# Kernel tuning notes

Measured on AMD Instinct MI355X. Metric: run time of the kernel, lower is better.

Reference implementation:

```python
import jax, jax.numpy as jnp
import numpy as np

DIM = 1024
HEADS = 16
HEAD_DIM = DIM // HEADS
MLP_DIM = 4096
EPS = 1e-12  # F.normalize eps


def l2_rms(x, g):
    # repo RMSNorm: F.normalize(x, dim=-1) * sqrt(d) * g  (g is a scalar param)
    d = x.shape[-1]
    n = jnp.sqrt(jnp.sum(x * x, axis=-1, keepdims=True))
    return x / jnp.maximum(n, EPS) * (d ** 0.5) * g


def setup_inputs() -> dict:
    key = jax.random.key(0)
    ks = jax.random.split(key, 8)
    B, N = 2, 2048
    s = lambda fan_in: 1.0 / np.sqrt(fan_in)
    return {
        "x": jax.random.normal(ks[0], (B, N, DIM), jnp.float32),
        "w_qkv": jax.random.normal(ks[1], (DIM, 3 * DIM), jnp.float32) * s(DIM),
        "b_qkv": jnp.zeros((3 * DIM,), jnp.float32),
        "w_proj": jax.random.normal(ks[2], (DIM, DIM), jnp.float32) * s(DIM),
        "b_proj": jnp.zeros((DIM,), jnp.float32),
        "g_norm1": jnp.ones((1,), jnp.float32),
        "g_norm2": jnp.ones((1,), jnp.float32),
        "g_qnorm": jnp.ones((1,), jnp.float32),
        "g_knorm": jnp.ones((1,), jnp.float32),
        "w_fc1": jax.random.normal(ks[3], (DIM, MLP_DIM), jnp.float32) * s(DIM),
        "b_fc1": jnp.zeros((MLP_DIM,), jnp.float32),
        "w_fc2": jax.random.normal(ks[4], (MLP_DIM, DIM), jnp.float32) * s(MLP_DIM),
        "b_fc2": jnp.zeros((DIM,), jnp.float32),
    }


def reference(x, w_qkv, b_qkv, w_proj, b_proj, g_norm1, g_norm2,
              g_qnorm, g_knorm, w_fc1, b_fc1, w_fc2, b_fc2):
    B, N, D = x.shape
    # --- attention branch ---
    h = l2_rms(x, g_norm1)
    qkv = h @ w_qkv + b_qkv                      # [B,N,3D]
    qkv = qkv.reshape(B, N, 3, HEADS, HEAD_DIM)
    q, k, v = [jnp.transpose(qkv[:, :, i], (0, 2, 1, 3)) for i in range(3)]  # [B,H,N,d]
    q = l2_rms(q, g_qnorm)
    k = l2_rms(k, g_knorm)
    scale = HEAD_DIM ** -0.5
    scores = jnp.einsum('bhqd,bhkd->bhqk', q * scale, k)   # explicit [B,H,N,N]
    attn = jax.nn.softmax(scores, axis=-1)
    o = jnp.einsum('bhqk,bhkd->bhqd', attn, v)
    o = jnp.transpose(o, (0, 2, 1, 3)).reshape(B, N, D)
    x = x + (o @ w_proj + b_proj)
    # --- MLP branch ---
    h = l2_rms(x, g_norm2)
    h = jax.nn.gelu(h @ w_fc1 + b_fc1, approximate=True)
    x = x + (h @ w_fc2 + b_fc2)
    return x
```

## Files before the change

kernel.cpp:

```cpp
#include <hip/hip_runtime.h>
#include <stdint.h>

#define SEQ_ 2048
#define DIM_ 1024
#define HD_ 64
#define NH_ 16

typedef __bf16 bf16x8 __attribute__((ext_vector_type(8)));
typedef float f32x4 __attribute__((ext_vector_type(4)));
typedef __attribute__((address_space(1))) unsigned int as1_uint;
typedef __attribute__((address_space(3))) unsigned int as3_uint;

__device__ __forceinline__ unsigned short f2bf(float f) {
  unsigned u = __builtin_bit_cast(unsigned, f);
  u += 0x7fffu + ((u >> 16) & 1u);
  return (unsigned short)(u >> 16);
}
__device__ __forceinline__ float bf2f(unsigned short u) {
  return __builtin_bit_cast(float, ((unsigned)u) << 16);
}
__device__ __forceinline__ unsigned pk_bf2(float lo, float hi) {
  return __builtin_amdgcn_perm(__builtin_bit_cast(unsigned, hi),
                               __builtin_bit_cast(unsigned, lo), 0x07060302u);
}

__device__ __forceinline__ void gload_lds16(const void* g, void* l) {
  __builtin_amdgcn_global_load_lds(
      reinterpret_cast<as1_uint*>(reinterpret_cast<uintptr_t>(g)),
      reinterpret_cast<as3_uint*>(
          static_cast<unsigned int>(reinterpret_cast<uintptr_t>(l))),
      16, 0, 0);
}

__global__ __launch_bounds__(256) void transpose_cvt(
    const float* __restrict__ W, unsigned short* __restrict__ Wt, int K, int N) {
  __shared__ float t[32][33];
  const int tx = threadIdx.x & 31, ty = threadIdx.x >> 5;
  const int n0 = blockIdx.x * 32, k0 = blockIdx.y * 32;
#pragma unroll
  for (int i = 0; i < 4; i++)
    t[ty + i * 8][tx] = W[(size_t)(k0 + ty + i * 8) * N + n0 + tx];
  __syncthreads();
#pragma unroll
  for (int i = 0; i < 4; i++)
    Wt[(size_t)(n0 + ty + i * 8) * K + k0 + tx] = f2bf(t[tx][ty + i * 8]);
}

__global__ __launch_bounds__(256) void rmsnorm_k(
    const float* __restrict__ x, const float* __restrict__ g,
    unsigned short* __restrict__ out) {
  const int row = blockIdx.x;
  const float4* xr = (const float4*)(x + (size_t)row * DIM_);
  float4 v = xr[threadIdx.x];
  float ss = v.x * v.x + v.y * v.y + v.z * v.z + v.w * v.w;
  ss += __shfl_xor(ss, 1);  ss += __shfl_xor(ss, 2);  ss += __shfl_xor(ss, 4);
  ss += __shfl_xor(ss, 8);  ss += __shfl_xor(ss, 16); ss += __shfl_xor(ss, 32);
  __shared__ float red[4];
  if ((threadIdx.x & 63) == 0) red[threadIdx.x >> 6] = ss;
  __syncthreads();
  float tot = red[0] + red[1] + red[2] + red[3];
  float sc = 32.0f * g[0] / fmaxf(sqrtf(tot), 1e-12f);
  unsigned short* orow = out + (size_t)row * DIM_;
  const int b4 = threadIdx.x * 4;
  orow[b4 + 0] = f2bf(v.x * sc);
  orow[b4 + 1] = f2bf(v.y * sc);
  orow[b4 + 2] = f2bf(v.z * sc);
  orow[b4 + 3] = f2bf(v.w * sc);
}

template <int EPI>
__global__ __launch_bounds__(256, 2) void gemm_bf16(
    const unsigned short* __restrict__ A, const unsigned short* __restrict__ Bt,
    const float* __restrict__ bias, const float* __restrict__ res,
    void* __restrict__ Cout, int M, int N, int K) {
  __shared__ __align__(16) unsigned short As[128 * 32];
  __shared__ __align__(16) unsigned short Bs[128 * 32];
  const int tid = threadIdx.x;
  const int w = tid >> 6, lane = tid & 63;
  const int wm = w >> 1, wn = w & 1;
  const int quad = lane >> 4, l15 = lane & 15;
  const int bn = blockIdx.x, bm = blockIdx.y;
  const int Kchunk = K / gridDim.z;
  const int kbeg = blockIdx.z * Kchunk;

  f32x4 acc[4][4];
#pragma unroll
  for (int i = 0; i < 4; i++)
#pragma unroll
    for (int j = 0; j < 4; j++) acc[i][j] = f32x4{0.f, 0.f, 0.f, 0.f};

  const int r0 = w * 16 + (lane >> 2);
  const int c0 = (lane & 3) * 8;
  const unsigned short* gA0 = A + (size_t)(bm * 128 + r0) * K + kbeg + c0;
  const unsigned short* gA1 = gA0 + (size_t)64 * K;
  const unsigned short* gB0 = Bt + (size_t)(bn * 128 + r0) * K + kbeg + c0;
  const unsigned short* gB1 = gB0 + (size_t)64 * K;
  unsigned short* lA0 = As + w * 512;
  unsigned short* lA1 = As + 2048 + w * 512;
  unsigned short* lB0 = Bs + w * 512;
  unsigned short* lB1 = Bs + 2048 + w * 512;

  for (int kk = 0; kk < Kchunk; kk += 32) {
    gload_lds16(gA0, lA0);
    gload_lds16(gA1, lA1);
    gload_lds16(gB0, lB0);
    gload_lds16(gB1, lB1);
    gA0 += 32; gA1 += 32; gB0 += 32; gB1 += 32;
    __syncthreads();
    bf16x8 af[4], bf[4];
#pragma unroll
    for (int i = 0; i < 4; i++) {
      af[i] = *(const bf16x8*)&As[(wm * 64 + i * 16 + l15) * 32 + quad * 8];
      bf[i] = *(const bf16x8*)&Bs[(wn * 64 + i * 16 + l15) * 32 + quad * 8];
    }
#pragma unroll
    for (int i = 0; i < 4; i++)
#pragma unroll
      for (int j = 0; j < 4; j++)
        acc[i][j] = __builtin_amdgcn_mfma_f32_16x16x32_bf16(af[i], bf[j], acc[i][j], 0, 0, 0);
    __syncthreads();
  }

  const int rowb = bm * 128 + wm * 64;
  const int colb = bn * 128 + wn * 64;
  float* Cz = (float*)Cout + (size_t)blockIdx.z * M * N;
#pragma unroll
  for (int i = 0; i < 4; i++) {
#pragma unroll
    for (int j = 0; j < 4; j++) {
      const int col = colb + j * 16 + l15;
      const float bv = (EPI == 3) ? 0.0f : bias[col];
#pragma unroll
      for (int r = 0; r < 4; r++) {
        const int row = rowb + i * 16 + quad * 4 + r;
        const size_t idx = (size_t)row * N + col;
        float v = acc[i][j][r] + bv;
        if (EPI == 0) {
          ((unsigned short*)Cout)[idx] = f2bf(v);
        } else if (EPI == 1) {
          ((float*)Cout)[idx] = v + res[idx];
        } else if (EPI == 2) {
          float t = tanhf(0.7978845608028654f * (v + 0.044715f * v * v * v));
          ((unsigned short*)Cout)[idx] = f2bf(0.5f * v * (1.0f + t));
        } else {
          Cz[idx] = v;
        }
      }
    }
  }
}

__global__ __launch_bounds__(256) void reduce_splitk(
    const float* __restrict__ part, int S, const float* __restrict__ res,
    const float* __restrict__ bias, float* __restrict__ out, int N, size_t MN) {
  const size_t n4 = MN >> 2;
  const size_t i = (size_t)blockIdx.x * 256 + threadIdx.x;
  if (i >= n4) return;
  float4 a = ((const float4*)res)[i];
  float4 b = ((const float4*)bias)[i % (size_t)(N >> 2)];
  float sx = a.x + b.x, sy = a.y + b.y, sz = a.z + b.z, sw = a.w + b.w;
  for (int z = 0; z < S; z++) {
    float4 p = ((const float4*)part)[z * n4 + i];
    sx += p.x; sy += p.y; sz += p.z; sw += p.w;
  }
  ((float4*)out)[i] = make_float4(sx, sy, sz, sw);
}

__global__ __launch_bounds__(256) void qkv_post(
    const unsigned short* __restrict__ qkv, const float* __restrict__ gq,
    const float* __restrict__ gk, unsigned short* __restrict__ Qs,
    unsigned short* __restrict__ Ks, unsigned short* __restrict__ VT) {
  const int item = blockIdx.x * 4 + (threadIdx.x >> 6);
  const int lane = threadIdx.x & 63;
  const int h = item & 15;
  const int rn = item >> 4;
  const int b = rn >> 11, n = rn & 2047;
  const unsigned short* base = qkv + (size_t)rn * 3072 + h * 64;
  const float qv = bf2f(base[lane]);
  const float kv = bf2f(base[1024 + lane]);
  const float vv = bf2f(base[2048 + lane]);
  float sq = qv * qv, sk = kv * kv;
  sq += __shfl_xor(sq, 1);  sk += __shfl_xor(sk, 1);
  sq += __shfl_xor(sq, 2);  sk += __shfl_xor(sk, 2);
  sq += __shfl_xor(sq, 4);  sk += __shfl_xor(sk, 4);
  sq += __shfl_xor(sq, 8);  sk += __shfl_xor(sk, 8);
  sq += __shfl_xor(sq, 16); sk += __shfl_xor(sk, 16);
  sq += __shfl_xor(sq, 32); sk += __shfl_xor(sk, 32);
  const float qs = qv / fmaxf(sqrtf(sq), 1e-12f) * gq[0];
  const float ks = kv / fmaxf(sqrtf(sk), 1e-12f) * (8.0f * gk[0]);
  const int bh = b * 16 + h;
  Qs[((size_t)bh * SEQ_ + n) * HD_ + lane] = f2bf(qs);
  Ks[((size_t)bh * SEQ_ + n) * HD_ + lane] = f2bf(ks);
  VT[((size_t)bh * HD_ + lane) * SEQ_ + n] = f2bf(vv);
}

#define PLD_ 72
__global__ __launch_bounds__(256) void attn_fwd(
    const unsigned short* __restrict__ Qs, const unsigned short* __restrict__ Ks,
    const unsigned short* __restrict__ VT, const float* __restrict__ gq,
    const float* __restrict__ gk, unsigned short* __restrict__ O) {
  __shared__ __align__(16) unsigned short Kl[2][64][32];
  __shared__ __align__(16) unsigned short Vl[2][64][32];
  __shared__ __align__(16) unsigned short Pl[4][16 * PLD_];
  const int bh = blockIdx.x, qt = blockIdx.y;
  const int w = threadIdx.x >> 6, lane = threadIdx.x & 63;
  const int quad = lane >> 4, l15 = lane & 15;
  const float M = 8.0f * fabsf(gq[0] * gk[0]);
  const unsigned short* Qb = Qs + (size_t)bh * SEQ_ * HD_;
  const unsigned short* Kb = Ks + (size_t)bh * SEQ_ * HD_;
  const unsigned short* Vb = VT + (size_t)bh * HD_ * SEQ_;
  const int q0 = qt * 64 + w * 16;
  const bf16x8 qa0 = *(const bf16x8*)&Qb[(q0 + l15) * HD_ + quad * 8];
  const bf16x8 qa1 = *(const bf16x8*)&Qb[(q0 + l15) * HD_ + 32 + quad * 8];

  const unsigned short* gsrc[4];
  unsigned short* ldst[4];
  int gstep[4];
#pragma unroll
  for (int i = 0; i < 4; i++) {
    const int idx = w * 4 + i;
    if (idx < 8) {
      const int kc = idx >> 2, kh = idx & 3;
      ldst[i] = &Kl[kc][kh * 16][0];
      gsrc[i] = &Kb[(size_t)(kh * 16 + (lane >> 2)) * HD_ + kc * 32 + (lane & 3) * 8];
      gstep[i] = 64 * HD_;
    } else {
      const int j = idx - 8;
      const int kc = j >> 2, dh = j & 3;
      ldst[i] = &Vl[kc][dh * 16][0];
      gsrc[i] = &Vb[(size_t)(dh * 16 + (lane >> 2)) * SEQ_ + kc * 32 + (lane & 3) * 8];
      gstep[i] = 64;
    }
  }

  f32x4 o[4];
  float lacc = 0.0f;
#pragma unroll
  for (int c = 0; c < 4; c++) o[c] = f32x4{0.f, 0.f, 0.f, 0.f};
  unsigned short* Pw = &Pl[w][0];

  for (int kt = 0; kt < SEQ_ / 64; kt++) {
#pragma unroll
    for (int i = 0; i < 4; i++) {
      gload_lds16(gsrc[i], ldst[i]);
      gsrc[i] += gstep[i];
    }
    __syncthreads();
    f32x4 st[4];
#pragma unroll
    for (int kn = 0; kn < 4; kn++) {
      const bf16x8 kf0 = *(const bf16x8*)&Kl[0][kn * 16 + l15][quad * 8];
      const bf16x8 kf1 = *(const bf16x8*)&Kl[1][kn * 16 + l15][quad * 8];
      st[kn] = __builtin_amdgcn_mfma_f32_16x16x32_bf16(kf0, qa0, f32x4{0.f, 0.f, 0.f, 0.f}, 0, 0, 0);
      st[kn] = __builtin_amdgcn_mfma_f32_16x16x32_bf16(kf1, qa1, st[kn], 0, 0, 0);
    }
#pragma unroll
    for (int kn = 0; kn < 4; kn++) {
      const float p0 = __expf(st[kn][0] - M);
      const float p1 = __expf(st[kn][1] - M);
      const float p2 = __expf(st[kn][2] - M);
      const float p3 = __expf(st[kn][3] - M);
      lacc += (p0 + p1) + (p2 + p3);
      uint2 pk;
      pk.x = pk_bf2(p0, p1);
      pk.y = pk_bf2(p2, p3);
      *(uint2*)&Pw[l15 * PLD_ + kn * 16 + quad * 4] = pk;
    }
    asm volatile("s_waitcnt lgkmcnt(0)" ::: "memory");
    const bf16x8 pa0 = *(const bf16x8*)&Pw[l15 * PLD_ + quad * 8];
    const bf16x8 pa1 = *(const bf16x8*)&Pw[l15 * PLD_ + 32 + quad * 8];
#pragma unroll
    for (int c = 0; c < 4; c++) {
      const bf16x8 vf0 = *(const bf16x8*)&Vl[0][c * 16 + l15][quad * 8];
      const bf16x8 vf1 = *(const bf16x8*)&Vl[1][c * 16 + l15][quad * 8];
      o[c] = __builtin_amdgcn_mfma_f32_16x16x32_bf16(pa0, vf0, o[c], 0, 0, 0);
      o[c] = __builtin_amdgcn_mfma_f32_16x16x32_bf16(pa1, vf1, o[c], 0, 0, 0);
    }
    __syncthreads();
  }

  lacc += __shfl_xor(lacc, 16);
  lacc += __shfl_xor(lacc, 32);
  const float linv = 1.0f / lacc;
  float lr[4];
#pragma unroll
  for (int r = 0; r < 4; r++) lr[r] = __shfl(linv, quad * 4 + r);
  const int b = bh >> 4, h = bh & 15;
#pragma unroll
  for (int c = 0; c < 4; c++)
#pragma unroll
    for (int r = 0; r < 4; r++) {
      const int row = q0 + quad * 4 + r;
      O[((size_t)(b * SEQ_ + row)) * DIM_ + h * 64 + c * 16 + l15] =
          f2bf(o[c][r] * lr[r]);
    }
}

extern "C" void kernel_launch(void* const* d_in, const int* in_sizes, int n_in,
                              void* d_out, int out_size, void* d_ws, size_t ws_size,
                              hipStream_t stream) {
  const float* x      = (const float*)d_in[0];
  const float* w_qkv  = (const float*)d_in[1];
  const float* b_qkv  = (const float*)d_in[2];
  const float* w_proj = (const float*)d_in[3];
  const float* b_proj = (const float*)d_in[4];
  const float* g1     = (const float*)d_in[5];
  const float* g2     = (const float*)d_in[6];
  const float* gq     = (const float*)d_in[7];
  const float* gk     = (const float*)d_in[8];
  const float* w_fc1  = (const float*)d_in[9];
  const float* b_fc1  = (const float*)d_in[10];
  const float* w_fc2  = (const float*)d_in[11];
  const float* b_fc2  = (const float*)d_in[12];
  float* out = (float*)d_out;

  char* p = (char*)d_ws;
  auto alloc = [&](size_t bytes) {
    char* r = p;
    p += (bytes + 255) & ~(size_t)255;
    return r;
  };
  const size_t MB = 1ull << 20;
  unsigned short* wqkvT  = (unsigned short*)alloc(3072ull * 1024 * 2);
  unsigned short* wprojT = (unsigned short*)alloc(1024ull * 1024 * 2);
  unsigned short* wfc1T  = (unsigned short*)alloc(4096ull * 1024 * 2);
  unsigned short* wfc2T  = (unsigned short*)alloc(1024ull * 4096 * 2);
  unsigned short* h1     = (unsigned short*)alloc(4096ull * 1024 * 2);
  unsigned short* QsB = (unsigned short*)alloc(32ull * SEQ_ * HD_ * 2);
  unsigned short* KsB = (unsigned short*)alloc(32ull * SEQ_ * HD_ * 2);
  unsigned short* VTB = (unsigned short*)alloc(32ull * SEQ_ * HD_ * 2);
  float* x2 = (float*)alloc(4096ull * 1024 * 4);
  unsigned short* h2 = (unsigned short*)alloc(4096ull * 1024 * 2);
  char* big = p;
  const size_t rem = ws_size - (size_t)(p - (char*)d_ws);
  unsigned short* qkvb = (unsigned short*)big;
  unsigned short* h3   = (unsigned short*)big;
  float* proj_part = (float*)big;
  float* fc2_part  = (float*)(big + 32 * MB);
  const int S_pr  = rem >= 64 * MB ? 2 : 1;
  const int S_fc2 = rem >= 96 * MB ? 4 : (rem >= 64 * MB ? 2 : 1);
  unsigned short* Obuf = h1;
  const size_t MN = 4096ull * 1024;

  transpose_cvt<<<dim3(3072 / 32, 1024 / 32), 256, 0, stream>>>(w_qkv, wqkvT, 1024, 3072);
  transpose_cvt<<<dim3(1024 / 32, 1024 / 32), 256, 0, stream>>>(w_proj, wprojT, 1024, 1024);
  transpose_cvt<<<dim3(4096 / 32, 1024 / 32), 256, 0, stream>>>(w_fc1, wfc1T, 1024, 4096);
  transpose_cvt<<<dim3(1024 / 32, 4096 / 32), 256, 0, stream>>>(w_fc2, wfc2T, 4096, 1024);
  rmsnorm_k<<<4096, 256, 0, stream>>>(x, g1, h1);
  gemm_bf16<0><<<dim3(3072 / 128, 4096 / 128), 256, 0, stream>>>(
      h1, wqkvT, b_qkv, nullptr, qkvb, 4096, 3072, 1024);
  qkv_post<<<16384, 256, 0, stream>>>(qkvb, gq, gk, QsB, KsB, VTB);
  attn_fwd<<<dim3(32, 32), 256, 0, stream>>>(QsB, KsB, VTB, gq, gk, Obuf);
  if (S_pr > 1) {
    gemm_bf16<3><<<dim3(1024 / 128, 4096 / 128, S_pr), 256, 0, stream>>>(
        Obuf, wprojT, b_proj, nullptr, proj_part, 4096, 1024, 1024);
    reduce_splitk<<<(MN / 4 + 255) / 256, 256, 0, stream>>>(
        proj_part, S_pr, x, b_proj, x2, 1024, MN);
  } else {
    gemm_bf16<1><<<dim3(1024 / 128, 4096 / 128), 256, 0, stream>>>(
        Obuf, wprojT, b_proj, x, x2, 4096, 1024, 1024);
  }
  rmsnorm_k<<<4096, 256, 0, stream>>>(x2, g2, h2);
  gemm_bf16<2><<<dim3(4096 / 128, 4096 / 128), 256, 0, stream>>>(
      h2, wfc1T, b_fc1, nullptr, h3, 4096, 4096, 1024);
  if (S_fc2 > 1) {
    gemm_bf16<3><<<dim3(1024 / 128, 4096 / 128, S_fc2), 256, 0, stream>>>(
        h3, wfc2T, b_fc2, nullptr, fc2_part, 4096, 1024, 4096);
    reduce_splitk<<<(MN / 4 + 255) / 256, 256, 0, stream>>>(
        fc2_part, S_fc2, x2, b_fc2, out, 1024, MN);
  } else {
    gemm_bf16<1><<<dim3(1024 / 128, 4096 / 128), 256, 0, stream>>>(
        h3, wfc2T, b_fc2, x2, out, 4096, 1024, 4096);
  }
}
```

Baseline: 414.4 us.

## Double-buffer attention K/V loads, merge weight transposes, fuse split-K reduce with RMSNorm

The attention kernel now double-buffers K/V tiles in LDS, issuing the next tile's global-to-LDS loads before computing on the current one and dropping the trailing barrier. The four weight transpose launches are merged into one launch. The proj split-K reduction is fused with the second RMSNorm, so x2 is not re-read. This costs twice the K/V LDS, and the single barrier per iteration must still guard buffer reuse correctly.

```diff
diff --git a/kernel.cpp b/kernel.cpp
--- a/kernel.cpp
+++ b/kernel.cpp
@@ -32,11 +32,21 @@
       16, 0, 0);
 }
 
-__global__ __launch_bounds__(256) void transpose_cvt(
-    const float* __restrict__ W, unsigned short* __restrict__ Wt, int K, int N) {
+__global__ __launch_bounds__(256) void transpose_all(
+    const float* __restrict__ w_qkv, const float* __restrict__ w_proj,
+    const float* __restrict__ w_fc1, const float* __restrict__ w_fc2,
+    unsigned short* __restrict__ o_qkv, unsigned short* __restrict__ o_proj,
+    unsigned short* __restrict__ o_fc1, unsigned short* __restrict__ o_fc2) {
+  int bid = blockIdx.x;
+  const float* W; unsigned short* Wt; int K, N;
+  if (bid < 3072)      { W = w_qkv;  Wt = o_qkv;  K = 1024; N = 3072; }
+  else if (bid < 4096) { W = w_proj; Wt = o_proj; K = 1024; N = 1024; bid -= 3072; }
+  else if (bid < 8192) { W = w_fc1;  Wt = o_fc1;  K = 1024; N = 4096; bid -= 4096; }
+  else                 { W = w_fc2;  Wt = o_fc2;  K = 4096; N = 1024; bid -= 8192; }
+  const int nx = N >> 5;
+  const int n0 = (bid % nx) * 32, k0 = (bid / nx) * 32;
   __shared__ float t[32][33];
   const int tx = threadIdx.x & 31, ty = threadIdx.x >> 5;
-  const int n0 = blockIdx.x * 32, k0 = blockIdx.y * 32;
 #pragma unroll
   for (int i = 0; i < 4; i++)
     t[ty + i * 8][tx] = W[(size_t)(k0 + ty + i * 8) * N + n0 + tx];
@@ -164,6 +174,37 @@
     sx += p.x; sy += p.y; sz += p.z; sw += p.w;
   }
   ((float4*)out)[i] = make_float4(sx, sy, sz, sw);
+}
+
+__global__ __launch_bounds__(256) void reduce_rms(
+    const float* __restrict__ part, int S, const float* __restrict__ res,
+    const float* __restrict__ bias, const float* __restrict__ g,
+    float* __restrict__ x2, unsigned short* __restrict__ h2) {
+  const int row = blockIdx.x;
+  const int t = threadIdx.x;
+  const size_t base = (size_t)row * DIM_;
+  float4 v = ((const float4*)(res + base))[t];
+  float4 b = ((const float4*)bias)[t];
+  v.x += b.x; v.y += b.y; v.z += b.z; v.w += b.w;
+  for (int z = 0; z < S; z++) {
+    float4 p = ((const float4*)(part + (size_t)z * SEQ_ * 2 * DIM_ + base))[t];
+    v.x += p.x; v.y += p.y; v.z += p.z; v.w += p.w;
+  }
+  ((float4*)(x2 + base))[t] = v;
+  float ss = v.x * v.x + v.y * v.y + v.z * v.z + v.w * v.w;
+  ss += __shfl_xor(ss, 1);  ss += __shfl_xor(ss, 2);  ss += __shfl_xor(ss, 4);
+  ss += __shfl_xor(ss, 8);  ss += __shfl_xor(ss, 16); ss += __shfl_xor(ss, 32);
+  __shared__ float red[4];
+  if ((t & 63) == 0) red[t >> 6] = ss;
+  __syncthreads();
+  const float tot = red[0] + red[1] + red[2] + red[3];
+  const float sc = 32.0f * g[0] / fmaxf(sqrtf(tot), 1e-12f);
+  unsigned short* orow = h2 + base;
+  const int b4 = t * 4;
+  orow[b4 + 0] = f2bf(v.x * sc);
+  orow[b4 + 1] = f2bf(v.y * sc);
+  orow[b4 + 2] = f2bf(v.z * sc);
+  orow[b4 + 3] = f2bf(v.w * sc);
 }
 
 __global__ __launch_bounds__(256) void qkv_post(
@@ -199,8 +240,8 @@
     const unsigned short* __restrict__ Qs, const unsigned short* __restrict__ Ks,
     const unsigned short* __restrict__ VT, const float* __restrict__ gq,
     const float* __restrict__ gk, unsigned short* __restrict__ O) {
-  __shared__ __align__(16) unsigned short Kl[2][64][32];
-  __shared__ __align__(16) unsigned short Vl[2][64][32];
+  __shared__ __align__(16) unsigned short Kl[2][2][64][32];
+  __shared__ __align__(16) unsigned short Vl[2][2][64][32];
   __shared__ __align__(16) unsigned short Pl[4][16 * PLD_];
   const int bh = blockIdx.x, qt = blockIdx.y;
   const int w = threadIdx.x >> 6, lane = threadIdx.x & 63;
@@ -214,20 +255,22 @@
   const bf16x8 qa1 = *(const bf16x8*)&Qb[(q0 + l15) * HD_ + 32 + quad * 8];
 
   const unsigned short* gsrc[4];
-  unsigned short* ldst[4];
+  unsigned short* ldst[2][4];
   int gstep[4];
 #pragma unroll
   for (int i = 0; i < 4; i++) {
     const int idx = w * 4 + i;
     if (idx < 8) {
       const int kc = idx >> 2, kh = idx & 3;
-      ldst[i] = &Kl[kc][kh * 16][0];
+      ldst[0][i] = &Kl[0][kc][kh * 16][0];
+      ldst[1][i] = &Kl[1][kc][kh * 16][0];
       gsrc[i] = &Kb[(size_t)(kh * 16 + (lane >> 2)) * HD_ + kc * 32 + (lane & 3) * 8];
       gstep[i] = 64 * HD_;
     } else {
       const int j = idx - 8;
       const int kc = j >> 2, dh = j & 3;
-      ldst[i] = &Vl[kc][dh * 16][0];
+      ldst[0][i] = &Vl[0][kc][dh * 16][0];
+      ldst[1][i] = &Vl[1][kc][dh * 16][0];
       gsrc[i] = &Vb[(size_t)(dh * 16 + (lane >> 2)) * SEQ_ + kc * 32 + (lane & 3) * 8];
       gstep[i] = 64;
     }
@@ -239,18 +282,27 @@
   for (int c = 0; c < 4; c++) o[c] = f32x4{0.f, 0.f, 0.f, 0.f};
   unsigned short* Pw = &Pl[w][0];
 
+#pragma unroll
+  for (int i = 0; i < 4; i++) {
+    gload_lds16(gsrc[i], ldst[0][i]);
+    gsrc[i] += gstep[i];
+  }
+
   for (int kt = 0; kt < SEQ_ / 64; kt++) {
-#pragma unroll
-    for (int i = 0; i < 4; i++) {
-      gload_lds16(gsrc[i], ldst[i]);
-      gsrc[i] += gstep[i];
-    }
+    const int cb = kt & 1;
     __syncthreads();
+    if (kt + 1 < SEQ_ / 64) {
+#pragma unroll
+      for (int i = 0; i < 4; i++) {
+        gload_lds16(gsrc[i], ldst[(kt + 1) & 1][i]);
+        gsrc[i] += gstep[i];
+      }
+    }
     f32x4 st[4];
 #pragma unroll
     for (int kn = 0; kn < 4; kn++) {
-      const bf16x8 kf0 = *(const bf16x8*)&Kl[0][kn * 16 + l15][quad * 8];
-      const bf16x8 kf1 = *(const bf16x8*)&Kl[1][kn * 16 + l15][quad * 8];
+      const bf16x8 kf0 = *(const bf16x8*)&Kl[cb][0][kn * 16 + l15][quad * 8];
+      const bf16x8 kf1 = *(const bf16x8*)&Kl[cb][1][kn * 16 + l15][quad * 8];
       st[kn] = __builtin_amdgcn_mfma_f32_16x16x32_bf16(kf0, qa0, f32x4{0.f, 0.f, 0.f, 0.f}, 0, 0, 0);
       st[kn] = __builtin_amdgcn_mfma_f32_16x16x32_bf16(kf1, qa1, st[kn], 0, 0, 0);
     }
@@ -271,12 +323,11 @@
     const bf16x8 pa1 = *(const bf16x8*)&Pw[l15 * PLD_ + 32 + quad * 8];
 #pragma unroll
     for (int c = 0; c < 4; c++) {
-      const bf16x8 vf0 = *(const bf16x8*)&Vl[0][c * 16 + l15][quad * 8];
-      const bf16x8 vf1 = *(const bf16x8*)&Vl[1][c * 16 + l15][quad * 8];
+      const bf16x8 vf0 = *(const bf16x8*)&Vl[cb][0][c * 16 + l15][quad * 8];
+      const bf16x8 vf1 = *(const bf16x8*)&Vl[cb][1][c * 16 + l15][quad * 8];
       o[c] = __builtin_amdgcn_mfma_f32_16x16x32_bf16(pa0, vf0, o[c], 0, 0, 0);
       o[c] = __builtin_amdgcn_mfma_f32_16x16x32_bf16(pa1, vf1, o[c], 0, 0, 0);
     }
-    __syncthreads();
   }
 
   lacc += __shfl_xor(lacc, 16);
@@ -342,10 +393,8 @@
   unsigned short* Obuf = h1;
   const size_t MN = 4096ull * 1024;
 
-  transpose_cvt<<<dim3(3072 / 32, 1024 / 32), 256, 0, stream>>>(w_qkv, wqkvT, 1024, 3072);
-  transpose_cvt<<<dim3(1024 / 32, 1024 / 32), 256, 0, stream>>>(w_proj, wprojT, 1024, 1024);
-  transpose_cvt<<<dim3(4096 / 32, 1024 / 32), 256, 0, stream>>>(w_fc1, wfc1T, 1024, 4096);
-  transpose_cvt<<<dim3(1024 / 32, 4096 / 32), 256, 0, stream>>>(w_fc2, wfc2T, 4096, 1024);
+  transpose_all<<<12288, 256, 0, stream>>>(w_qkv, w_proj, w_fc1, w_fc2,
+                                           wqkvT, wprojT, wfc1T, wfc2T);
   rmsnorm_k<<<4096, 256, 0, stream>>>(x, g1, h1);
   gemm_bf16<0><<<dim3(3072 / 128, 4096 / 128), 256, 0, stream>>>(
       h1, wqkvT, b_qkv, nullptr, qkvb, 4096, 3072, 1024);
@@ -354,13 +403,12 @@
   if (S_pr > 1) {
     gemm_bf16<3><<<dim3(1024 / 128, 4096 / 128, S_pr), 256, 0, stream>>>(
         Obuf, wprojT, b_proj, nullptr, proj_part, 4096, 1024, 1024);
-    reduce_splitk<<<(MN / 4 + 255) / 256, 256, 0, stream>>>(
-        proj_part, S_pr, x, b_proj, x2, 1024, MN);
+    reduce_rms<<<4096, 256, 0, stream>>>(proj_part, S_pr, x, b_proj, g2, x2, h2);
   } else {
     gemm_bf16<1><<<dim3(1024 / 128, 4096 / 128), 256, 0, stream>>>(
         Obuf, wprojT, b_proj, x, x2, 4096, 1024, 1024);
-  }
-  rmsnorm_k<<<4096, 256, 0, stream>>>(x2, g2, h2);
+    rmsnorm_k<<<4096, 256, 0, stream>>>(x2, g2, h2);
+  }
   gemm_bf16<2><<<dim3(4096 / 128, 4096 / 128), 256, 0, stream>>>(
       h2, wfc1T, b_fc1, nullptr, h3, 4096, 4096, 1024);
   if (S_fc2 > 1) {
```

After: 420.3 us. Within noise of the previous version (+1.4%).
